# Kernel tuning notes

Hardware: AMD Instinct MI355X
Metric: run time of the kernel (lower is better)

Reference implementation:

```python
import jax, jax.numpy as jnp
import numpy as np

N_NODES = 50000


def gcn_conv(x, W, b, src, dst, ew, n_nodes):
    """PyG GCNConv: out = D^{-1/2}(A + I)D^{-1/2} (x @ W) + b, A weighted by ew.

    Self loops (weight 1) are handled analytically instead of appending edges.
    """
    h = x @ W  # [N, out]
    # degree includes self-loop weight of 1
    deg = jax.ops.segment_sum(ew, dst, num_segments=n_nodes) + 1.0  # [N]
    dinv = jnp.where(deg > 0, jax.lax.rsqrt(deg), 0.0)
    norm = dinv[src] * ew * dinv[dst]  # [E]
    # message = norm * h[src], scatter-add to dst
    agg = jax.ops.segment_sum(h[src] * norm[:, None], dst, num_segments=n_nodes)
    # self-loop contribution: dinv[i] * 1 * dinv[i] * h[i]
    agg = agg + h * (dinv * dinv)[:, None]
    return agg + b


def setup_inputs() -> dict:
    key = jax.random.key(0)
    k = jax.random.split(key, 8)
    n, e, d_in, d_h = N_NODES, 600000, 128, 128
    x = jax.random.normal(k[0], (n, d_in), dtype=jnp.float32)
    edge_index = jax.random.randint(k[1], (2, e), 0, n, dtype=jnp.int64)
    edge_attr = jax.random.uniform(k[2], (e,), dtype=jnp.float32)
    s1 = 1.0 / np.sqrt(d_in)
    s2 = 1.0 / np.sqrt(d_h)
    W1 = jax.random.uniform(k[3], (d_in, d_h), jnp.float32, -s1, s1)
    b1 = jnp.zeros((d_h,), jnp.float32)
    W2 = jax.random.uniform(k[4], (d_h, d_h), jnp.float32, -s2, s2)
    b2 = jnp.zeros((d_h,), jnp.float32)
    return {"x": x, "edge_index": edge_index, "edge_attr": edge_attr,
            "W1": W1, "b1": b1, "W2": W2, "b2": b2}


def reference(x, edge_index, edge_attr, W1, b1, W2, b2):
    src, dst = edge_index[0], edge_index[1]
    h = gcn_conv(x, W1, b1, src, dst, edge_attr, N_NODES)
    h = jax.nn.relu(h)
    # dropout is identity in eval mode (deterministic reference)
    out = gcn_conv(h, W2, b2, src, dst, edge_attr, N_NODES)
    return out
```

## Files before the change

### kernel.cpp

```cpp
#include <hip/hip_runtime.h>
#include <stdint.h>

#define D 128
#define EPB 4096
#define CSZ 128

typedef __bf16 bf16x8 __attribute__((ext_vector_type(8)));
typedef float f32x4 __attribute__((ext_vector_type(4)));

__device__ inline float bf2f(unsigned short u) {
    return __uint_as_float((unsigned)u << 16);
}
__device__ inline unsigned short f2bf(float f) {
    unsigned u = __float_as_uint(f);
    return (unsigned short)((u + 0x7FFF + ((u >> 16) & 1)) >> 16);
}

struct Params {
    const float* x; const int* ei; const float* ew;
    const float* W1; const float* b1; const float* W2; const float* b2;
    float* out;
    int N, E, C, B1n, total, gb, hb, sb;
    unsigned short *Wt1, *Wt2;
    unsigned int* bh; int* ebase; int* bsums;
    float* dinv; int* cnt; int* rowstart;
    int2* brec; int2* erec;
    unsigned short *Hbuf, *Abuf;
};


__device__ inline void dev_prep(int which, const Params& p) {
    const float* W = (which == 0) ? p.W1 : p.W2;
    unsigned short* Wt = (which == 0) ? p.Wt1 : p.Wt2;
    for (int i = threadIdx.x; i < 2048; i += 256) {
        int nn = i >> 4;
        int kc = (i & 15) << 3;
        ushort4 o0, o1;
        o0.x = f2bf(W[(kc + 0) * 128 + nn]); o0.y = f2bf(W[(kc + 1) * 128 + nn]);
        o0.z = f2bf(W[(kc + 2) * 128 + nn]); o0.w = f2bf(W[(kc + 3) * 128 + nn]);
        o1.x = f2bf(W[(kc + 4) * 128 + nn]); o1.y = f2bf(W[(kc + 5) * 128 + nn]);
        o1.z = f2bf(W[(kc + 6) * 128 + nn]); o1.w = f2bf(W[(kc + 7) * 128 + nn]);
        *(ushort4*)(Wt + nn * 128 + kc) = o0;
        *(ushort4*)(Wt + nn * 128 + kc + 4) = o1;
    }
}

__device__ inline void dev_hist(int b, const Params& p, unsigned int* hist) {
    for (int i = threadIdx.x; i < p.C; i += 256) hist[i] = 0;
    __syncthreads();
    const int base = b * EPB + threadIdx.x;
#pragma unroll
    for (int k = 0; k < EPB / 256; ++k) {
        int e = base + k * 256;
        if (e < p.E) atomicAdd(&hist[((unsigned)p.ei[p.E + e]) >> 7], 1u);
    }
    __syncthreads();
    for (int i = threadIdx.x; i < p.C; i += 256) p.bh[(size_t)b * p.C + i] = hist[i];
}

__device__ inline void dev_scanA(int blk, const Params& p, int* tmp) {
    const int tid = threadIdx.x;
    const int i = blk * 256 + tid;
    int v = 0;
    if (i < p.total) {
        int c = i / p.B1n;
        int b = i - c * p.B1n;
        v = (int)p.bh[(size_t)b * p.C + c];
    }
    tmp[tid] = v;
    __syncthreads();
    for (int off = 1; off < 256; off <<= 1) {
        int t = (tid >= off) ? tmp[tid - off] : 0;
        __syncthreads();
        tmp[tid] += t;
        __syncthreads();
    }
    if (i < p.total) p.ebase[i] = tmp[tid] - v;
    if (tid == 255) p.bsums[blk] = tmp[255];
}

__device__ inline void dev_scanB(int blk, const Params& p, int* sred) {
    const int tid = threadIdx.x;
    int v = (tid < blk) ? p.bsums[tid] : 0;
#pragma unroll
    for (int off = 32; off; off >>= 1) v += __shfl_down(v, off);
    if ((tid & 63) == 0) sred[tid >> 6] = v;
    __syncthreads();
    int tot = sred[0] + sred[1] + sred[2] + sred[3];
    int i = blk * 256 + tid;
    if (i < p.total) p.ebase[i] += tot;
}

__device__ inline void dev_scat(int b, const Params& p, unsigned int* cur) {
    for (int i = threadIdx.x; i < p.C; i += 256) cur[i] = 0;
    __syncthreads();
    const int base = b * EPB + threadIdx.x;
#pragma unroll
    for (int k = 0; k < EPB / 256; ++k) {
        int e = base + k * 256;
        if (e < p.E) {
            int s = p.ei[e];
            unsigned d = (unsigned)p.ei[p.E + e];
            float w = p.ew[e];
            int c = d >> 7;
            unsigned r = atomicAdd(&cur[c], 1u);
            int pos = p.ebase[c * p.B1n + b] + (int)r;
            p.brec[pos] = make_int2((int)((d << 16) | (unsigned)s), __float_as_int(w));
        }
    }
}

__device__ inline void dev_cbuild(int c, const Params& p, unsigned int* a) {
    unsigned int* hcnt = a;
    unsigned int* hdeg = a + CSZ;
    unsigned int* lsc  = a + 2 * CSZ;
    unsigned int* curs = a + 3 * CSZ;
    const int tid = threadIdx.x;
    const int cs = p.ebase[c * p.B1n];
    const int ce = (c + 1 < p.C) ? p.ebase[(c + 1) * p.B1n] : p.E;
    if (tid < CSZ) { hcnt[tid] = 0; hdeg[tid] = 0; }
    __syncthreads();
    for (int i = cs + tid; i < ce; i += 256) {
        int2 r = p.brec[i];
        int local = (int)(((unsigned)r.x) >> 16) & (CSZ - 1);
        atomicAdd(&hcnt[local], 1u);
        atomicAdd(&hdeg[local], (unsigned)(__int_as_float(r.y) * 16777216.0f));
    }
    __syncthreads();
    if (tid < CSZ) lsc[tid] = hcnt[tid];
    __syncthreads();
    for (int off = 1; off < CSZ; off <<= 1) {
        unsigned t = (tid < CSZ && tid >= off) ? lsc[tid - off] : 0u;
        __syncthreads();
        if (tid < CSZ) lsc[tid] += t;
        __syncthreads();
    }
    if (tid < CSZ) {
        unsigned excl = lsc[tid] - hcnt[tid];
        curs[tid] = excl;
        int node = c * CSZ + tid;
        if (node < p.N) {
            p.rowstart[node] = cs + (int)excl;
            p.cnt[node] = (int)hcnt[tid];
            float deg = 1.0f + (float)hdeg[tid] * (1.0f / 16777216.0f);
            p.dinv[node] = rsqrtf(deg);
        }
    }
    __syncthreads();
    for (int i = cs + tid; i < ce; i += 256) {
        int2 r = p.brec[i];
        int local = (int)(((unsigned)r.x) >> 16) & (CSZ - 1);
        unsigned rk = atomicAdd(&curs[local], 1u);
        p.erec[cs + (int)rk] = make_int2(r.x & 0xFFFF, r.y);
    }
}

template <bool IN_BF16>
__device__ inline void mfma_body(unsigned short* sE,
                                 const void* __restrict__ Xv,
                                 const unsigned short* __restrict__ Wt,
                                 unsigned short* __restrict__ H, int n, int blk) {
    const int tid = threadIdx.x;
    const int row0 = blk * 64;
    const int lane = tid & 63;
    const int wv = tid >> 6;
    const int qm = lane & 15;
    const int quad = lane >> 4;

    const int arow = row0 + wv * 16 + qm;
    const int ar = (arow < n) ? arow : (n - 1);

    f32x4 acc[8];
#pragma unroll
    for (int i = 0; i < 8; ++i) acc[i] = (f32x4){0.f, 0.f, 0.f, 0.f};

#pragma unroll
    for (int kb = 0; kb < 4; ++kb) {
        const int koff = kb * 32 + quad * 8;
        bf16x8 a;
        if (IN_BF16) {
            a = *(const bf16x8*)((const unsigned short*)Xv + (size_t)ar * 128 + koff);
        } else {
            const float* Xf = (const float*)Xv + (size_t)ar * 128 + koff;
            float4 v0 = *(const float4*)(Xf);
            float4 v1 = *(const float4*)(Xf + 4);
            union { bf16x8 v; ushort4 u[2]; } cv;
            cv.u[0].x = f2bf(v0.x); cv.u[0].y = f2bf(v0.y);
            cv.u[0].z = f2bf(v0.z); cv.u[0].w = f2bf(v0.w);
            cv.u[1].x = f2bf(v1.x); cv.u[1].y = f2bf(v1.y);
            cv.u[1].z = f2bf(v1.z); cv.u[1].w = f2bf(v1.w);
            a = cv.v;
        }
#pragma unroll
        for (int n0 = 0; n0 < 8; ++n0) {
            bf16x8 b = *(const bf16x8*)(Wt + (n0 * 16 + qm) * 128 + koff);
            acc[n0] = __builtin_amdgcn_mfma_f32_16x16x32_bf16(a, b, acc[n0], 0, 0, 0);
        }
    }

#pragma unroll
    for (int n0 = 0; n0 < 8; ++n0)
#pragma unroll
        for (int r = 0; r < 4; ++r)
            sE[(wv * 16 + quad * 4 + r) * 136 + n0 * 16 + qm] = f2bf(acc[n0][r]);
    __syncthreads();

    const int row_in = lane >> 2;
    const int c0 = (lane & 3) * 4;
    const int grow = row0 + wv * 16 + row_in;
    if (grow < n) {
#pragma unroll
        for (int j = 0; j < 4; ++j)
            *(int4*)(H + (size_t)grow * 128 + (c0 + j) * 8) =
                *(const int4*)(&sE[(wv * 16 + row_in) * 136 + (c0 + j) * 8]);
    }
}

template <bool OUT_BF16>
__device__ inline void gather_body(const Params& p, const ushort4* __restrict__ H4,
                                   const float4* __restrict__ bias4,
                                   void* __restrict__ OUTv, int g) {
    const int lane = threadIdx.x & 31;
    const int node = g * 8 + (threadIdx.x >> 5);
    if (node >= p.N) return;
    const int start = p.rowstart[node];
    const int m = p.cnt[node];
    const float di = p.dinv[node];

    float4 b = bias4[lane];
    ushort4 h = H4[(size_t)node * 32 + lane];
    float ax = di * bf2f(h.x);
    float ay = di * bf2f(h.y);
    float az = di * bf2f(h.z);
    float aw = di * bf2f(h.w);

    int j = 0;
    for (; j + 4 <= m; j += 4) {
        const int base = start + j;
        int2 e0 = p.erec[base + 0], e1 = p.erec[base + 1];
        int2 e2 = p.erec[base + 2], e3 = p.erec[base + 3];
        float w0 = p.dinv[e0.x] * __int_as_float(e0.y);
        float w1 = p.dinv[e1.x] * __int_as_float(e1.y);
        float w2 = p.dinv[e2.x] * __int_as_float(e2.y);
        float w3 = p.dinv[e3.x] * __int_as_float(e3.y);
        ushort4 v0 = H4[(size_t)e0.x * 32 + lane];
        ushort4 v1 = H4[(size_t)e1.x * 32 + lane];
        ushort4 v2 = H4[(size_t)e2.x * 32 + lane];
        ushort4 v3 = H4[(size_t)e3.x * 32 + lane];
        ax += w0 * bf2f(v0.x); ay += w0 * bf2f(v0.y); az += w0 * bf2f(v0.z); aw += w0 * bf2f(v0.w);
        ax += w1 * bf2f(v1.x); ay += w1 * bf2f(v1.y); az += w1 * bf2f(v1.z); aw += w1 * bf2f(v1.w);
        ax += w2 * bf2f(v2.x); ay += w2 * bf2f(v2.y); az += w2 * bf2f(v2.z); aw += w2 * bf2f(v2.w);
        ax += w3 * bf2f(v3.x); ay += w3 * bf2f(v3.y); az += w3 * bf2f(v3.z); aw += w3 * bf2f(v3.w);
    }
    for (; j < m; ++j) {
        int2 er = p.erec[start + j];
        float w = p.dinv[er.x] * __int_as_float(er.y);
        ushort4 v = H4[(size_t)er.x * 32 + lane];
        ax += w * bf2f(v.x); ay += w * bf2f(v.y); az += w * bf2f(v.z); aw += w * bf2f(v.w);
    }
    ax = b.x + di * ax; ay = b.y + di * ay;
    az = b.z + di * az; aw = b.w + di * aw;
    if (OUT_BF16) {
        ushort4 o;
        o.x = f2bf(fmaxf(ax, 0.f)); o.y = f2bf(fmaxf(ay, 0.f));
        o.z = f2bf(fmaxf(az, 0.f)); o.w = f2bf(fmaxf(aw, 0.f));
        ((ushort4*)OUTv)[(size_t)node * 32 + lane] = o;
    } else {
        float4 o; o.x = ax; o.y = ay; o.z = az; o.w = aw;
        ((float4*)OUTv)[(size_t)node * 32 + lane] = o;
    }
}

__global__ __launch_bounds__(256, 4) void k_f0(Params p) {
    __shared__ __align__(16) char arena[64 * 136 * 2];
    if (blockIdx.x < 2) dev_prep(blockIdx.x, p);
    else dev_hist(blockIdx.x - 2, p, (unsigned int*)arena);
}
__global__ __launch_bounds__(256, 4) void k_f1(Params p) {
    __shared__ __align__(16) char arena[64 * 136 * 2];
    if ((int)blockIdx.x < p.gb) mfma_body<false>((unsigned short*)arena, (const void*)p.x, p.Wt1, p.Hbuf, p.N, blockIdx.x);
    else dev_scanA(blockIdx.x - p.gb, p, (int*)arena);
}
__global__ __launch_bounds__(256) void k_f2(Params p) {
    __shared__ int sred[4];
    dev_scanB(blockIdx.x, p, sred);
}
__global__ __launch_bounds__(256) void k_f3(Params p) {
    __shared__ unsigned int cur[512];
    dev_scat(blockIdx.x, p, cur);
}
__global__ __launch_bounds__(256) void k_f4(Params p) {
    __shared__ unsigned int a[4 * CSZ];
    dev_cbuild(blockIdx.x, p, a);
}
__global__ __launch_bounds__(256) void k_f5(Params p) {
    gather_body<true>(p, (const ushort4*)p.Hbuf, (const float4*)p.b1, (void*)p.Abuf, blockIdx.x);
}
__global__ __launch_bounds__(256, 4) void k_f6(Params p) {
    __shared__ __align__(16) char arena[64 * 136 * 2];
    mfma_body<true>((unsigned short*)arena, (const void*)p.Abuf, p.Wt2, p.Hbuf, p.N, blockIdx.x);
}
__global__ __launch_bounds__(256) void k_f7(Params p) {
    gather_body<false>(p, (const ushort4*)p.Hbuf, (const float4*)p.b2, (void*)p.out, blockIdx.x);
}

extern "C" void kernel_launch(void* const* d_in, const int* in_sizes, int n_in,
                              void* d_out, int out_size, void* d_ws, size_t ws_size,
                              hipStream_t stream) {
    Params p;
    p.x  = (const float*)d_in[0];
    p.ei = (const int*)d_in[1];
    p.ew = (const float*)d_in[2];
    p.W1 = (const float*)d_in[3];
    p.b1 = (const float*)d_in[4];
    p.W2 = (const float*)d_in[5];
    p.b2 = (const float*)d_in[6];
    p.out = (float*)d_out;

    p.N = in_sizes[0] / D;
    p.E = in_sizes[2];
    p.C = (p.N + CSZ - 1) / CSZ;
    p.B1n = (p.E + EPB - 1) / EPB;
    p.total = p.C * p.B1n;
    p.sb = (p.total + 255) / 256;
    p.gb = (p.N + 63) / 64;
    p.hb = (p.N + 7) / 8;

    char* w = (char*)d_ws;
    auto alloc = [&](size_t bytes) {
        void* r = (void*)w;
        w += (bytes + 255) & ~(size_t)255;
        return r;
    };
    p.bh       = (unsigned int*)alloc((size_t)p.total * 4);
    p.ebase    = (int*)alloc((size_t)p.total * 4);
    p.bsums    = (int*)alloc(1024 * 4);
    p.dinv     = (float*)alloc((size_t)p.N * 4);
    p.cnt      = (int*)alloc((size_t)p.N * 4);
    p.rowstart = (int*)alloc((size_t)p.N * 4);
    p.brec     = (int2*)alloc((size_t)p.E * 8);
    p.erec     = (int2*)alloc((size_t)p.E * 8);
    p.Hbuf     = (unsigned short*)alloc((size_t)p.N * D * 2);
    p.Abuf     = (unsigned short*)alloc((size_t)p.N * D * 2);
    p.Wt1      = (unsigned short*)alloc(128 * 128 * 2);
    p.Wt2      = (unsigned short*)alloc(128 * 128 * 2);

    k_f0<<<2 + p.B1n, 256, 0, stream>>>(p);
    k_f1<<<p.gb + p.sb, 256, 0, stream>>>(p);
    k_f2<<<p.sb, 256, 0, stream>>>(p);
    k_f3<<<p.B1n, 256, 0, stream>>>(p);
    k_f4<<<p.C, 256, 0, stream>>>(p);
    k_f5<<<p.hb, 256, 0, stream>>>(p);
    k_f6<<<p.gb, 256, 0, stream>>>(p);
    k_f7<<<p.hb, 256, 0, stream>>>(p);
}
```

Baseline: 218.8 us.

## Fuse all GCN stages into one cooperative persistent kernel with grid syncs

Replaces the eight separate kernel launches with a single cooperative kernel that loops over work units per stage and separates stages with grid-wide barriers. The bucketing step is rebuilt around a global per-chunk counter, a scan in a single block, and atomic cursor allocation, which removes the large per-block histogram scan. The goal is to cut launch gaps and the cost of the multi-pass scan. In exchange it adds grid.sync overhead, a fixed persistent grid size, and non-deterministic edge ordering inside each bucket. The old launch sequence stays as a fallback if the cooperative launch fails.

```diff
diff --git a/kernel.cpp b/kernel.cpp
--- a/kernel.cpp
+++ b/kernel.cpp
@@ -1,8 +1,12 @@
 #include <hip/hip_runtime.h>
+#include <hip/hip_cooperative_groups.h>
 #include <stdint.h>
+
+namespace cg = cooperative_groups;
 
 #define D 128
 #define EPB 4096
+#define EPB2 1024
 #define CSZ 128
 
 typedef __bf16 bf16x8 __attribute__((ext_vector_type(8)));
@@ -20,9 +24,10 @@
     const float* x; const int* ei; const float* ew;
     const float* W1; const float* b1; const float* W2; const float* b2;
     float* out;
-    int N, E, C, B1n, total, gb, hb, sb;
+    int N, E, C, B1n, B2n, total, gb, hb, sb;
     unsigned short *Wt1, *Wt2;
     unsigned int* bh; int* ebase; int* bsums;
+    unsigned int* ctot; int* cbase; unsigned int* gcur;
     float* dinv; int* cnt; int* rowstart;
     int2* brec; int2* erec;
     unsigned short *Hbuf, *Abuf;
@@ -110,14 +115,78 @@
     }
 }
 
-__device__ inline void dev_cbuild(int c, const Params& p, unsigned int* a) {
+__device__ inline void dev_hist2(int b, const Params& p, unsigned int* hist) {
+    for (int i = threadIdx.x; i < p.C; i += 256) hist[i] = 0;
+    __syncthreads();
+    const int base = b * EPB2 + threadIdx.x;
+#pragma unroll
+    for (int k = 0; k < EPB2 / 256; ++k) {
+        int e = base + k * 256;
+        if (e < p.E) atomicAdd(&hist[((unsigned)p.ei[p.E + e]) >> 7], 1u);
+    }
+    __syncthreads();
+    for (int i = threadIdx.x; i < p.C; i += 256) {
+        unsigned v = hist[i];
+        if (v) atomicAdd(&p.ctot[i], v);
+    }
+}
+
+__device__ inline void dev_cscan(const Params& p, int* s) {
+    const int tid = threadIdx.x;
+    const int c0 = tid, c1 = tid + 256;
+    s[c0] = (c0 < p.C) ? (int)p.ctot[c0] : 0;
+    s[c1] = (c1 < p.C) ? (int)p.ctot[c1] : 0;
+    __syncthreads();
+    for (int off = 1; off < 512; off <<= 1) {
+        int t0 = (c0 >= off) ? s[c0 - off] : 0;
+        int t1 = (c1 >= off) ? s[c1 - off] : 0;
+        __syncthreads();
+        s[c0] += t0; s[c1] += t1;
+        __syncthreads();
+    }
+    if (c0 < p.C) { int b0 = (c0 == 0) ? 0 : s[c0 - 1]; p.cbase[c0] = b0; p.gcur[c0] = (unsigned)b0; }
+    if (c1 < p.C) { int b1 = s[c1 - 1]; p.cbase[c1] = b1; p.gcur[c1] = (unsigned)b1; }
+    if (tid == 0) p.cbase[p.C] = p.E;
+}
+
+__device__ inline void dev_scat2(int b, const Params& p, unsigned int* a) {
+    unsigned int* hcnt = a;
+    unsigned int* hcur = a + 512;
+    const int tid = threadIdx.x;
+    for (int i = tid; i < p.C; i += 256) hcnt[i] = 0;
+    __syncthreads();
+    const int base = b * EPB2 + tid;
+#pragma unroll
+    for (int k = 0; k < EPB2 / 256; ++k) {
+        int e = base + k * 256;
+        if (e < p.E) atomicAdd(&hcnt[((unsigned)p.ei[p.E + e]) >> 7], 1u);
+    }
+    __syncthreads();
+    for (int i = tid; i < p.C; i += 256) {
+        unsigned c = hcnt[i];
+        hcur[i] = c ? atomicAdd(&p.gcur[i], c) : 0u;
+    }
+    __syncthreads();
+#pragma unroll
+    for (int k = 0; k < EPB2 / 256; ++k) {
+        int e = base + k * 256;
+        if (e < p.E) {
+            int s = p.ei[e];
+            unsigned d = (unsigned)p.ei[p.E + e];
+            float w = p.ew[e];
+            int c = (int)(d >> 7);
+            unsigned r = atomicAdd(&hcur[c], 1u);
+            p.brec[r] = make_int2((int)((d << 16) | (unsigned)s), __float_as_int(w));
+        }
+    }
+}
+
+__device__ inline void dev_cbuild(int c, const Params& p, unsigned int* a, int cs, int ce) {
     unsigned int* hcnt = a;
     unsigned int* hdeg = a + CSZ;
     unsigned int* lsc  = a + 2 * CSZ;
     unsigned int* curs = a + 3 * CSZ;
     const int tid = threadIdx.x;
-    const int cs = p.ebase[c * p.B1n];
-    const int ce = (c + 1 < p.C) ? p.ebase[(c + 1) * p.B1n] : p.E;
     if (tid < CSZ) { hcnt[tid] = 0; hdeg[tid] = 0; }
     __syncthreads();
     for (int i = cs + tid; i < ce; i += 256) {
@@ -222,53 +291,99 @@
                                    void* __restrict__ OUTv, int g) {
     const int lane = threadIdx.x & 31;
     const int node = g * 8 + (threadIdx.x >> 5);
-    if (node >= p.N) return;
-    const int start = p.rowstart[node];
-    const int m = p.cnt[node];
-    const float di = p.dinv[node];
-
-    float4 b = bias4[lane];
-    ushort4 h = H4[(size_t)node * 32 + lane];
-    float ax = di * bf2f(h.x);
-    float ay = di * bf2f(h.y);
-    float az = di * bf2f(h.z);
-    float aw = di * bf2f(h.w);
-
-    int j = 0;
-    for (; j + 4 <= m; j += 4) {
-        const int base = start + j;
-        int2 e0 = p.erec[base + 0], e1 = p.erec[base + 1];
-        int2 e2 = p.erec[base + 2], e3 = p.erec[base + 3];
-        float w0 = p.dinv[e0.x] * __int_as_float(e0.y);
-        float w1 = p.dinv[e1.x] * __int_as_float(e1.y);
-        float w2 = p.dinv[e2.x] * __int_as_float(e2.y);
-        float w3 = p.dinv[e3.x] * __int_as_float(e3.y);
-        ushort4 v0 = H4[(size_t)e0.x * 32 + lane];
-        ushort4 v1 = H4[(size_t)e1.x * 32 + lane];
-        ushort4 v2 = H4[(size_t)e2.x * 32 + lane];
-        ushort4 v3 = H4[(size_t)e3.x * 32 + lane];
-        ax += w0 * bf2f(v0.x); ay += w0 * bf2f(v0.y); az += w0 * bf2f(v0.z); aw += w0 * bf2f(v0.w);
-        ax += w1 * bf2f(v1.x); ay += w1 * bf2f(v1.y); az += w1 * bf2f(v1.z); aw += w1 * bf2f(v1.w);
-        ax += w2 * bf2f(v2.x); ay += w2 * bf2f(v2.y); az += w2 * bf2f(v2.z); aw += w2 * bf2f(v2.w);
-        ax += w3 * bf2f(v3.x); ay += w3 * bf2f(v3.y); az += w3 * bf2f(v3.z); aw += w3 * bf2f(v3.w);
-    }
-    for (; j < m; ++j) {
-        int2 er = p.erec[start + j];
-        float w = p.dinv[er.x] * __int_as_float(er.y);
-        ushort4 v = H4[(size_t)er.x * 32 + lane];
-        ax += w * bf2f(v.x); ay += w * bf2f(v.y); az += w * bf2f(v.z); aw += w * bf2f(v.w);
-    }
-    ax = b.x + di * ax; ay = b.y + di * ay;
-    az = b.z + di * az; aw = b.w + di * aw;
-    if (OUT_BF16) {
-        ushort4 o;
-        o.x = f2bf(fmaxf(ax, 0.f)); o.y = f2bf(fmaxf(ay, 0.f));
-        o.z = f2bf(fmaxf(az, 0.f)); o.w = f2bf(fmaxf(aw, 0.f));
-        ((ushort4*)OUTv)[(size_t)node * 32 + lane] = o;
-    } else {
-        float4 o; o.x = ax; o.y = ay; o.z = az; o.w = aw;
-        ((float4*)OUTv)[(size_t)node * 32 + lane] = o;
-    }
+    if (node < p.N) {
+        const int start = p.rowstart[node];
+        const int m = p.cnt[node];
+        const float di = p.dinv[node];
+
+        float4 b = bias4[lane];
+        ushort4 h = H4[(size_t)node * 32 + lane];
+        float ax = di * bf2f(h.x);
+        float ay = di * bf2f(h.y);
+        float az = di * bf2f(h.z);
+        float aw = di * bf2f(h.w);
+
+        int j = 0;
+        for (; j + 4 <= m; j += 4) {
+            const int base = start + j;
+            int2 e0 = p.erec[base + 0], e1 = p.erec[base + 1];
+            int2 e2 = p.erec[base + 2], e3 = p.erec[base + 3];
+            float w0 = p.dinv[e0.x] * __int_as_float(e0.y);
+            float w1 = p.dinv[e1.x] * __int_as_float(e1.y);
+            float w2 = p.dinv[e2.x] * __int_as_float(e2.y);
+            float w3 = p.dinv[e3.x] * __int_as_float(e3.y);
+            ushort4 v0 = H4[(size_t)e0.x * 32 + lane];
+            ushort4 v1 = H4[(size_t)e1.x * 32 + lane];
+            ushort4 v2 = H4[(size_t)e2.x * 32 + lane];
+            ushort4 v3 = H4[(size_t)e3.x * 32 + lane];
+            ax += w0 * bf2f(v0.x); ay += w0 * bf2f(v0.y); az += w0 * bf2f(v0.z); aw += w0 * bf2f(v0.w);
+            ax += w1 * bf2f(v1.x); ay += w1 * bf2f(v1.y); az += w1 * bf2f(v1.z); aw += w1 * bf2f(v1.w);
+            ax += w2 * bf2f(v2.x); ay += w2 * bf2f(v2.y); az += w2 * bf2f(v2.z); aw += w2 * bf2f(v2.w);
+            ax += w3 * bf2f(v3.x); ay += w3 * bf2f(v3.y); az += w3 * bf2f(v3.z); aw += w3 * bf2f(v3.w);
+        }
+        for (; j < m; ++j) {
+            int2 er = p.erec[start + j];
+            float w = p.dinv[er.x] * __int_as_float(er.y);
+            ushort4 v = H4[(size_t)er.x * 32 + lane];
+            ax += w * bf2f(v.x); ay += w * bf2f(v.y); az += w * bf2f(v.z); aw += w * bf2f(v.w);
+        }
+        ax = b.x + di * ax; ay = b.y + di * ay;
+        az = b.z + di * az; aw = b.w + di * aw;
+        if (OUT_BF16) {
+            ushort4 o;
+            o.x = f2bf(fmaxf(ax, 0.f)); o.y = f2bf(fmaxf(ay, 0.f));
+            o.z = f2bf(fmaxf(az, 0.f)); o.w = f2bf(fmaxf(aw, 0.f));
+            ((ushort4*)OUTv)[(size_t)node * 32 + lane] = o;
+        } else {
+            float4 o; o.x = ax; o.y = ay; o.z = az; o.w = aw;
+            ((float4*)OUTv)[(size_t)node * 32 + lane] = o;
+        }
+    }
+}
+
+__global__ __launch_bounds__(256, 4) void k_all(Params p) {
+    __shared__ __align__(16) char arena[64 * 136 * 2];
+    cg::grid_group grid = cg::this_grid();
+    const int nb = (int)gridDim.x;
+
+    for (int u = blockIdx.x; u < 2 + p.B2n; u += nb) {
+        if (u < 2) dev_prep(u, p);
+        else dev_hist2(u - 2, p, (unsigned int*)arena);
+        __syncthreads();
+    }
+    grid.sync();
+
+    for (int u = blockIdx.x; u < p.gb + 1; u += nb) {
+        if (u < p.gb) mfma_body<false>((unsigned short*)arena, (const void*)p.x, p.Wt1, p.Hbuf, p.N, u);
+        else dev_cscan(p, (int*)arena);
+        __syncthreads();
+    }
+    grid.sync();
+
+    for (int u = blockIdx.x; u < p.B2n; u += nb) {
+        dev_scat2(u, p, (unsigned int*)arena);
+        __syncthreads();
+    }
+    grid.sync();
+
+    for (int u = blockIdx.x; u < p.C; u += nb) {
+        dev_cbuild(u, p, (unsigned int*)arena, p.cbase[u], p.cbase[u + 1]);
+        __syncthreads();
+    }
+    grid.sync();
+
+    for (int u = blockIdx.x; u < p.hb; u += nb)
+        gather_body<true>(p, (const ushort4*)p.Hbuf, (const float4*)p.b1, (void*)p.Abuf, u);
+    grid.sync();
+
+    for (int u = blockIdx.x; u < p.gb; u += nb) {
+        mfma_body<true>((unsigned short*)arena, (const void*)p.Abuf, p.Wt2, p.Hbuf, p.N, u);
+        __syncthreads();
+    }
+    grid.sync();
+
+    for (int u = blockIdx.x; u < p.hb; u += nb)
+        gather_body<false>(p, (const ushort4*)p.Hbuf, (const float4*)p.b2, (void*)p.out, u);
 }
 
 __global__ __launch_bounds__(256, 4) void k_f0(Params p) {
@@ -291,7 +406,10 @@
 }
 __global__ __launch_bounds__(256) void k_f4(Params p) {
     __shared__ unsigned int a[4 * CSZ];
-    dev_cbuild(blockIdx.x, p, a);
+    int c = blockIdx.x;
+    int cs = p.ebase[c * p.B1n];
+    int ce = (c + 1 < p.C) ? p.ebase[(c + 1) * p.B1n] : p.E;
+    dev_cbuild(c, p, a, cs, ce);
 }
 __global__ __launch_bounds__(256) void k_f5(Params p) {
     gather_body<true>(p, (const ushort4*)p.Hbuf, (const float4*)p.b1, (void*)p.Abuf, blockIdx.x);
@@ -321,6 +439,7 @@
     p.E = in_sizes[2];
     p.C = (p.N + CSZ - 1) / CSZ;
     p.B1n = (p.E + EPB - 1) / EPB;
+    p.B2n = (p.E + EPB2 - 1) / EPB2;
     p.total = p.C * p.B1n;
     p.sb = (p.total + 255) / 256;
     p.gb = (p.N + 63) / 64;
@@ -335,6 +454,9 @@
     p.bh       = (unsigned int*)alloc((size_t)p.total * 4);
     p.ebase    = (int*)alloc((size_t)p.total * 4);
     p.bsums    = (int*)alloc(1024 * 4);
+    p.ctot     = (unsigned int*)alloc((size_t)p.C * 4);
+    p.cbase    = (int*)alloc((size_t)(p.C + 1) * 4);
+    p.gcur     = (unsigned int*)alloc((size_t)p.C * 4);
     p.dinv     = (float*)alloc((size_t)p.N * 4);
     p.cnt      = (int*)alloc((size_t)p.N * 4);
     p.rowstart = (int*)alloc((size_t)p.N * 4);
@@ -345,12 +467,38 @@
     p.Wt1      = (unsigned short*)alloc(128 * 128 * 2);
     p.Wt2      = (unsigned short*)alloc(128 * 128 * 2);
 
-    k_f0<<<2 + p.B1n, 256, 0, stream>>>(p);
-    k_f1<<<p.gb + p.sb, 256, 0, stream>>>(p);
-    k_f2<<<p.sb, 256, 0, stream>>>(p);
-    k_f3<<<p.B1n, 256, 0, stream>>>(p);
-    k_f4<<<p.C, 256, 0, stream>>>(p);
-    k_f5<<<p.hb, 256, 0, stream>>>(p);
-    k_f6<<<p.gb, 256, 0, stream>>>(p);
-    k_f7<<<p.hb, 256, 0, stream>>>(p);
-}
+    bool fused_ok = (p.C <= 512);
+
+    static int s_grid = 0;
+    if (s_grid == 0) {
+        int ba = 0;
+        if (hipOccupancyMaxActiveBlocksPerMultiprocessor(&ba, (const void*)k_all, 256, 0) != hipSuccess || ba < 1)
+            ba = 2;
+        int ncu = 256;
+        hipDeviceProp_t prop;
+        int dev = 0;
+        if (hipGetDevice(&dev) == hipSuccess && hipGetDeviceProperties(&prop, dev) == hipSuccess &&
+            prop.multiProcessorCount > 0)
+            ncu = prop.multiProcessorCount;
+        long g = (long)ba * (long)ncu;
+        s_grid = (int)(g > 1024 ? 1024 : g);
+        if (s_grid < 64) s_grid = 64;
+    }
+
+    hipError_t err = hipErrorUnknown;
+    if (fused_ok) {
+        hipMemsetAsync(p.ctot, 0, (size_t)p.C * 4, stream);
+        void* kargs[] = { (void*)&p };
+        err = hipLaunchCooperativeKernel((const void*)k_all, dim3(s_grid), dim3(256), kargs, 0u, stream);
+    }
+    if (err != hipSuccess) {
+        k_f0<<<2 + p.B1n, 256, 0, stream>>>(p);
+        k_f1<<<p.gb + p.sb, 256, 0, stream>>>(p);
+        k_f2<<<p.sb, 256, 0, stream>>>(p);
+        k_f3<<<p.B1n, 256, 0, stream>>>(p);
+        k_f4<<<p.C, 256, 0, stream>>>(p);
+        k_f5<<<p.hb, 256, 0, stream>>>(p);
+        k_f6<<<p.gb, 256, 0, stream>>>(p);
+        k_f7<<<p.hb, 256, 0, stream>>>(p);
+    }
+}
```

New measurement: 680.9 us. 3.11x slower.

## Replace two-level bucket scan with global atomic cursors and fuse gather1 into GEMM2

Applied to the files above, without the earlier changes.

The per-block histogram scan (scanA/scanB, two launches) is replaced by per-bucket totals accumulated with global atomics, a single-block scan, and a scatter that reserves ranges through global atomic cursors. The scatter recounts its own edges to get its reservation. The first-layer aggregation now writes straight into LDS and feeds the second-layer MFMA GEMM in the same kernel, so the intermediate activation buffer no longer round-trips through global memory and two launches are removed. Edge order within a bucket now depends on atomic timing, so float sums are no longer deterministic. The fused kernel uses 8 threads per node, which may lower gather parallelism and occupancy.

```diff
diff --git a/kernel.cpp b/kernel.cpp
--- a/kernel.cpp
+++ b/kernel.cpp
@@ -2,7 +2,7 @@
 #include <stdint.h>
 
 #define D 128
-#define EPB 4096
+#define EPB2 1024
 #define CSZ 128
 
 typedef __bf16 bf16x8 __attribute__((ext_vector_type(8)));
@@ -20,12 +20,12 @@
     const float* x; const int* ei; const float* ew;
     const float* W1; const float* b1; const float* W2; const float* b2;
     float* out;
-    int N, E, C, B1n, total, gb, hb, sb;
+    int N, E, C, B2n, gb, hb;
     unsigned short *Wt1, *Wt2;
-    unsigned int* bh; int* ebase; int* bsums;
+    unsigned int* ctot; int* cbase; unsigned int* gcur;
     float* dinv; int* cnt; int* rowstart;
     int2* brec; int2* erec;
-    unsigned short *Hbuf, *Abuf;
+    unsigned short *Hbuf, *H2;
 };
 
 
@@ -45,79 +45,78 @@
     }
 }
 
-__device__ inline void dev_hist(int b, const Params& p, unsigned int* hist) {
+__device__ inline void dev_hist2(int b, const Params& p, unsigned int* hist) {
     for (int i = threadIdx.x; i < p.C; i += 256) hist[i] = 0;
     __syncthreads();
-    const int base = b * EPB + threadIdx.x;
-#pragma unroll
-    for (int k = 0; k < EPB / 256; ++k) {
+    const int base = b * EPB2 + threadIdx.x;
+#pragma unroll
+    for (int k = 0; k < EPB2 / 256; ++k) {
         int e = base + k * 256;
         if (e < p.E) atomicAdd(&hist[((unsigned)p.ei[p.E + e]) >> 7], 1u);
     }
     __syncthreads();
-    for (int i = threadIdx.x; i < p.C; i += 256) p.bh[(size_t)b * p.C + i] = hist[i];
-}
-
-__device__ inline void dev_scanA(int blk, const Params& p, int* tmp) {
-    const int tid = threadIdx.x;
-    const int i = blk * 256 + tid;
-    int v = 0;
-    if (i < p.total) {
-        int c = i / p.B1n;
-        int b = i - c * p.B1n;
-        v = (int)p.bh[(size_t)b * p.C + c];
-    }
-    tmp[tid] = v;
-    __syncthreads();
-    for (int off = 1; off < 256; off <<= 1) {
-        int t = (tid >= off) ? tmp[tid - off] : 0;
+    for (int i = threadIdx.x; i < p.C; i += 256) {
+        unsigned v = hist[i];
+        if (v) atomicAdd(&p.ctot[i], v);
+    }
+}
+
+__device__ inline void dev_cscan(const Params& p, int* s) {
+    const int tid = threadIdx.x;
+    const int c0 = tid, c1 = tid + 256;
+    s[c0] = (c0 < p.C) ? (int)p.ctot[c0] : 0;
+    s[c1] = (c1 < p.C) ? (int)p.ctot[c1] : 0;
+    __syncthreads();
+    for (int off = 1; off < 512; off <<= 1) {
+        int t0 = (c0 >= off) ? s[c0 - off] : 0;
+        int t1 = (c1 >= off) ? s[c1 - off] : 0;
         __syncthreads();
-        tmp[tid] += t;
+        s[c0] += t0; s[c1] += t1;
         __syncthreads();
     }
-    if (i < p.total) p.ebase[i] = tmp[tid] - v;
-    if (tid == 255) p.bsums[blk] = tmp[255];
-}
-
-__device__ inline void dev_scanB(int blk, const Params& p, int* sred) {
-    const int tid = threadIdx.x;
-    int v = (tid < blk) ? p.bsums[tid] : 0;
-#pragma unroll
-    for (int off = 32; off; off >>= 1) v += __shfl_down(v, off);
-    if ((tid & 63) == 0) sred[tid >> 6] = v;
-    __syncthreads();
-    int tot = sred[0] + sred[1] + sred[2] + sred[3];
-    int i = blk * 256 + tid;
-    if (i < p.total) p.ebase[i] += tot;
-}
-
-__device__ inline void dev_scat(int b, const Params& p, unsigned int* cur) {
-    for (int i = threadIdx.x; i < p.C; i += 256) cur[i] = 0;
-    __syncthreads();
-    const int base = b * EPB + threadIdx.x;
-#pragma unroll
-    for (int k = 0; k < EPB / 256; ++k) {
+    if (c0 < p.C) { int b0 = (c0 == 0) ? 0 : s[c0 - 1]; p.cbase[c0] = b0; p.gcur[c0] = (unsigned)b0; }
+    if (c1 < p.C) { int b1 = s[c1 - 1]; p.cbase[c1] = b1; p.gcur[c1] = (unsigned)b1; }
+    if (tid == 0) p.cbase[p.C] = p.E;
+}
+
+__device__ inline void dev_scat2(int b, const Params& p, unsigned int* a) {
+    unsigned int* hcnt = a;
+    unsigned int* hcur = a + 512;
+    const int tid = threadIdx.x;
+    for (int i = tid; i < p.C; i += 256) hcnt[i] = 0;
+    __syncthreads();
+    const int base = b * EPB2 + tid;
+#pragma unroll
+    for (int k = 0; k < EPB2 / 256; ++k) {
+        int e = base + k * 256;
+        if (e < p.E) atomicAdd(&hcnt[((unsigned)p.ei[p.E + e]) >> 7], 1u);
+    }
+    __syncthreads();
+    for (int i = tid; i < p.C; i += 256) {
+        unsigned c = hcnt[i];
+        hcur[i] = c ? atomicAdd(&p.gcur[i], c) : 0u;
+    }
+    __syncthreads();
+#pragma unroll
+    for (int k = 0; k < EPB2 / 256; ++k) {
         int e = base + k * 256;
         if (e < p.E) {
             int s = p.ei[e];
             unsigned d = (unsigned)p.ei[p.E + e];
             float w = p.ew[e];
-            int c = d >> 7;
-            unsigned r = atomicAdd(&cur[c], 1u);
-            int pos = p.ebase[c * p.B1n + b] + (int)r;
-            p.brec[pos] = make_int2((int)((d << 16) | (unsigned)s), __float_as_int(w));
-        }
-    }
-}
-
-__device__ inline void dev_cbuild(int c, const Params& p, unsigned int* a) {
+            int c = (int)(d >> 7);
+            unsigned r = atomicAdd(&hcur[c], 1u);
+            p.brec[r] = make_int2((int)((d << 16) | (unsigned)s), __float_as_int(w));
+        }
+    }
+}
+
+__device__ inline void dev_cbuild(int c, const Params& p, unsigned int* a, int cs, int ce) {
     unsigned int* hcnt = a;
     unsigned int* hdeg = a + CSZ;
     unsigned int* lsc  = a + 2 * CSZ;
     unsigned int* curs = a + 3 * CSZ;
     const int tid = threadIdx.x;
-    const int cs = p.ebase[c * p.B1n];
-    const int ce = (c + 1 < p.C) ? p.ebase[(c + 1) * p.B1n] : p.E;
     if (tid < CSZ) { hcnt[tid] = 0; hdeg[tid] = 0; }
     __syncthreads();
     for (int i = cs + tid; i < ce; i += 256) {
@@ -216,10 +215,81 @@
     }
 }
 
-template <bool OUT_BF16>
-__device__ inline void gather_body(const Params& p, const ushort4* __restrict__ H4,
-                                   const float4* __restrict__ bias4,
-                                   void* __restrict__ OUTv, int g) {
+__device__ inline void gather1_to_lds(const Params& p, unsigned short* sA, int row0) {
+    const int tid = threadIdx.x;
+    const int lane8 = tid & 7;
+    const int grp = tid >> 3;
+    const ushort4* __restrict__ H4 = (const ushort4*)p.Hbuf;
+#pragma unroll
+    for (int pass = 0; pass < 2; ++pass) {
+        const int local = pass * 32 + grp;
+        const int node = row0 + local;
+        unsigned short* dst = sA + local * 136 + lane8 * 16;
+        if (node < p.N) {
+            const int start = p.rowstart[node];
+            const int m = p.cnt[node];
+            const float di = p.dinv[node];
+            const ushort4* Hrow = H4 + (size_t)node * 32 + lane8 * 4;
+            float acc[16];
+#pragma unroll
+            for (int q = 0; q < 4; ++q) {
+                ushort4 h = Hrow[q];
+                acc[q * 4 + 0] = di * bf2f(h.x);
+                acc[q * 4 + 1] = di * bf2f(h.y);
+                acc[q * 4 + 2] = di * bf2f(h.z);
+                acc[q * 4 + 3] = di * bf2f(h.w);
+            }
+            int j = 0;
+            for (; j + 2 <= m; j += 2) {
+                int2 e0 = p.erec[start + j];
+                int2 e1 = p.erec[start + j + 1];
+                float w0 = p.dinv[e0.x] * __int_as_float(e0.y);
+                float w1 = p.dinv[e1.x] * __int_as_float(e1.y);
+                const ushort4* V0 = H4 + (size_t)e0.x * 32 + lane8 * 4;
+                const ushort4* V1 = H4 + (size_t)e1.x * 32 + lane8 * 4;
+#pragma unroll
+                for (int q = 0; q < 4; ++q) {
+                    ushort4 v0 = V0[q], v1 = V1[q];
+                    acc[q * 4 + 0] += w0 * bf2f(v0.x) + w1 * bf2f(v1.x);
+                    acc[q * 4 + 1] += w0 * bf2f(v0.y) + w1 * bf2f(v1.y);
+                    acc[q * 4 + 2] += w0 * bf2f(v0.z) + w1 * bf2f(v1.z);
+                    acc[q * 4 + 3] += w0 * bf2f(v0.w) + w1 * bf2f(v1.w);
+                }
+            }
+            if (j < m) {
+                int2 e0 = p.erec[start + j];
+                float w0 = p.dinv[e0.x] * __int_as_float(e0.y);
+                const ushort4* V0 = H4 + (size_t)e0.x * 32 + lane8 * 4;
+#pragma unroll
+                for (int q = 0; q < 4; ++q) {
+                    ushort4 v0 = V0[q];
+                    acc[q * 4 + 0] += w0 * bf2f(v0.x);
+                    acc[q * 4 + 1] += w0 * bf2f(v0.y);
+                    acc[q * 4 + 2] += w0 * bf2f(v0.z);
+                    acc[q * 4 + 3] += w0 * bf2f(v0.w);
+                }
+            }
+            const float* bb = p.b1 + lane8 * 16;
+#pragma unroll
+            for (int q = 0; q < 4; ++q) {
+                ushort4 o;
+                o.x = f2bf(fmaxf(bb[q * 4 + 0] + di * acc[q * 4 + 0], 0.f));
+                o.y = f2bf(fmaxf(bb[q * 4 + 1] + di * acc[q * 4 + 1], 0.f));
+                o.z = f2bf(fmaxf(bb[q * 4 + 2] + di * acc[q * 4 + 2], 0.f));
+                o.w = f2bf(fmaxf(bb[q * 4 + 3] + di * acc[q * 4 + 3], 0.f));
+                *(ushort4*)(dst + q * 4) = o;
+            }
+        } else {
+            ushort4 z = {0, 0, 0, 0};
+#pragma unroll
+            for (int q = 0; q < 4; ++q) *(ushort4*)(dst + q * 4) = z;
+        }
+    }
+}
+
+__device__ inline void gather2_body(const Params& p, const ushort4* __restrict__ H4,
+                                    const float4* __restrict__ bias4,
+                                    float4* __restrict__ OUT, int g) {
     const int lane = threadIdx.x & 31;
     const int node = g * 8 + (threadIdx.x >> 5);
     if (node >= p.N) return;
@@ -258,50 +328,77 @@
         ushort4 v = H4[(size_t)er.x * 32 + lane];
         ax += w * bf2f(v.x); ay += w * bf2f(v.y); az += w * bf2f(v.z); aw += w * bf2f(v.w);
     }
-    ax = b.x + di * ax; ay = b.y + di * ay;
-    az = b.z + di * az; aw = b.w + di * aw;
-    if (OUT_BF16) {
-        ushort4 o;
-        o.x = f2bf(fmaxf(ax, 0.f)); o.y = f2bf(fmaxf(ay, 0.f));
-        o.z = f2bf(fmaxf(az, 0.f)); o.w = f2bf(fmaxf(aw, 0.f));
-        ((ushort4*)OUTv)[(size_t)node * 32 + lane] = o;
-    } else {
-        float4 o; o.x = ax; o.y = ay; o.z = az; o.w = aw;
-        ((float4*)OUTv)[(size_t)node * 32 + lane] = o;
-    }
-}
-
-__global__ __launch_bounds__(256, 4) void k_f0(Params p) {
-    __shared__ __align__(16) char arena[64 * 136 * 2];
+    float4 o;
+    o.x = b.x + di * ax; o.y = b.y + di * ay;
+    o.z = b.z + di * az; o.w = b.w + di * aw;
+    OUT[(size_t)node * 32 + lane] = o;
+}
+
+__global__ __launch_bounds__(256, 4) void k_a0(Params p) {
+    __shared__ __align__(16) unsigned int hist[512];
     if (blockIdx.x < 2) dev_prep(blockIdx.x, p);
-    else dev_hist(blockIdx.x - 2, p, (unsigned int*)arena);
-}
-__global__ __launch_bounds__(256, 4) void k_f1(Params p) {
+    else dev_hist2(blockIdx.x - 2, p, hist);
+}
+__global__ __launch_bounds__(256, 4) void k_a1(Params p) {
     __shared__ __align__(16) char arena[64 * 136 * 2];
     if ((int)blockIdx.x < p.gb) mfma_body<false>((unsigned short*)arena, (const void*)p.x, p.Wt1, p.Hbuf, p.N, blockIdx.x);
-    else dev_scanA(blockIdx.x - p.gb, p, (int*)arena);
-}
-__global__ __launch_bounds__(256) void k_f2(Params p) {
-    __shared__ int sred[4];
-    dev_scanB(blockIdx.x, p, sred);
-}
-__global__ __launch_bounds__(256) void k_f3(Params p) {
-    __shared__ unsigned int cur[512];
-    dev_scat(blockIdx.x, p, cur);
-}
-__global__ __launch_bounds__(256) void k_f4(Params p) {
+    else dev_cscan(p, (int*)arena);
+}
+__global__ __launch_bounds__(256) void k_a2(Params p) {
+    __shared__ unsigned int a[1024];
+    dev_scat2(blockIdx.x, p, a);
+}
+__global__ __launch_bounds__(256) void k_a3(Params p) {
     __shared__ unsigned int a[4 * CSZ];
-    dev_cbuild(blockIdx.x, p, a);
-}
-__global__ __launch_bounds__(256) void k_f5(Params p) {
-    gather_body<true>(p, (const ushort4*)p.Hbuf, (const float4*)p.b1, (void*)p.Abuf, blockIdx.x);
-}
-__global__ __launch_bounds__(256, 4) void k_f6(Params p) {
-    __shared__ __align__(16) char arena[64 * 136 * 2];
-    mfma_body<true>((unsigned short*)arena, (const void*)p.Abuf, p.Wt2, p.Hbuf, p.N, blockIdx.x);
-}
-__global__ __launch_bounds__(256) void k_f7(Params p) {
-    gather_body<false>(p, (const ushort4*)p.Hbuf, (const float4*)p.b2, (void*)p.out, blockIdx.x);
+    dev_cbuild(blockIdx.x, p, a, p.cbase[blockIdx.x], p.cbase[blockIdx.x + 1]);
+}
+__global__ __launch_bounds__(256, 4) void k_a4(Params p) {
+    __shared__ __align__(16) unsigned short sA[64 * 136];
+    __shared__ __align__(16) unsigned short sE[64 * 136];
+    const int row0 = blockIdx.x * 64;
+    gather1_to_lds(p, sA, row0);
+    __syncthreads();
+
+    const int tid = threadIdx.x;
+    const int lane = tid & 63;
+    const int wv = tid >> 6;
+    const int qm = lane & 15;
+    const int quad = lane >> 4;
+
+    f32x4 acc[8];
+#pragma unroll
+    for (int i = 0; i < 8; ++i) acc[i] = (f32x4){0.f, 0.f, 0.f, 0.f};
+
+#pragma unroll
+    for (int kb = 0; kb < 4; ++kb) {
+        const int koff = kb * 32 + quad * 8;
+        bf16x8 a = *(const bf16x8*)(sA + (wv * 16 + qm) * 136 + koff);
+#pragma unroll
+        for (int n0 = 0; n0 < 8; ++n0) {
+            bf16x8 b = *(const bf16x8*)(p.Wt2 + (n0 * 16 + qm) * 128 + koff);
+            acc[n0] = __builtin_amdgcn_mfma_f32_16x16x32_bf16(a, b, acc[n0], 0, 0, 0);
+        }
+    }
+
+#pragma unroll
+    for (int n0 = 0; n0 < 8; ++n0)
+#pragma unroll
+        for (int r = 0; r < 4; ++r)
+            sE[(wv * 16 + quad * 4 + r) * 136 + n0 * 16 + qm] = f2bf(acc[n0][r]);
+    __syncthreads();
+
+    const int row_in = lane >> 2;
+    const int c0 = (lane & 3) * 4;
+    const int grow = row0 + wv * 16 + row_in;
+    if (grow < p.N) {
+#pragma unroll
+        for (int j = 0; j < 4; ++j)
+            *(int4*)(p.H2 + (size_t)grow * 128 + (c0 + j) * 8) =
+                *(const int4*)(&sE[(wv * 16 + row_in) * 136 + (c0 + j) * 8]);
+    }
+}
+__global__ __launch_bounds__(256) void k_a5(Params p) {
+    gather2_body(p, (const ushort4*)p.H2, (const float4*)p.b2, (float4*)p.out, blockIdx.x);
 }
 
 extern "C" void kernel_launch(void* const* d_in, const int* in_sizes, int n_in,
@@ -320,9 +417,7 @@
     p.N = in_sizes[0] / D;
     p.E = in_sizes[2];
     p.C = (p.N + CSZ - 1) / CSZ;
-    p.B1n = (p.E + EPB - 1) / EPB;
-    p.total = p.C * p.B1n;
-    p.sb = (p.total + 255) / 256;
+    p.B2n = (p.E + EPB2 - 1) / EPB2;
     p.gb = (p.N + 63) / 64;
     p.hb = (p.N + 7) / 8;
 
@@ -332,25 +427,24 @@
         w += (bytes + 255) & ~(size_t)255;
         return r;
     };
-    p.bh       = (unsigned int*)alloc((size_t)p.total * 4);
-    p.ebase    = (int*)alloc((size_t)p.total * 4);
-    p.bsums    = (int*)alloc(1024 * 4);
+    p.ctot     = (unsigned int*)alloc((size_t)p.C * 4);
+    p.cbase    = (int*)alloc((size_t)(p.C + 1) * 4);
+    p.gcur     = (unsigned int*)alloc((size_t)p.C * 4);
     p.dinv     = (float*)alloc((size_t)p.N * 4);
     p.cnt      = (int*)alloc((size_t)p.N * 4);
     p.rowstart = (int*)alloc((size_t)p.N * 4);
     p.brec     = (int2*)alloc((size_t)p.E * 8);
     p.erec     = (int2*)alloc((size_t)p.E * 8);
     p.Hbuf     = (unsigned short*)alloc((size_t)p.N * D * 2);
-    p.Abuf     = (unsigned short*)alloc((size_t)p.N * D * 2);
+    p.H2       = (unsigned short*)alloc((size_t)p.N * D * 2);
     p.Wt1      = (unsigned short*)alloc(128 * 128 * 2);
     p.Wt2      = (unsigned short*)alloc(128 * 128 * 2);
 
-    k_f0<<<2 + p.B1n, 256, 0, stream>>>(p);
-    k_f1<<<p.gb + p.sb, 256, 0, stream>>>(p);
-    k_f2<<<p.sb, 256, 0, stream>>>(p);
-    k_f3<<<p.B1n, 256, 0, stream>>>(p);
-    k_f4<<<p.C, 256, 0, stream>>>(p);
-    k_f5<<<p.hb, 256, 0, stream>>>(p);
-    k_f6<<<p.gb, 256, 0, stream>>>(p);
-    k_f7<<<p.hb, 256, 0, stream>>>(p);
-}
+    hipMemsetAsync(p.ctot, 0, (size_t)p.C * 4, stream);
+    k_a0<<<2 + p.B2n, 256, 0, stream>>>(p);
+    k_a1<<<p.gb + 1, 256, 0, stream>>>(p);
+    k_a2<<<p.B2n, 256, 0, stream>>>(p);
+    k_a3<<<p.C, 256, 0, stream>>>(p);
+    k_a4<<<p.gb, 256, 0, stream>>>(p);
+    k_a5<<<p.hb, 256, 0, stream>>>(p);
+}
```

After: 227.5 us. 1.04x slower.

## Replace two-level bucketed CSR build with per-node global atomic counting sort

Applied to the files above, without the earlier changes.

The two-pass bucket sort (per-block chunk histograms, two-level scan, bucket scatter, per-chunk local rebuild) is replaced by per-destination global atomics. One packed 64-bit atomic accumulates both edge count and degree per node, a per-node scan plus a single-block scan of block sums builds row offsets, and one scatter pass places edges through per-node atomic cursors. This removes the intermediate brec buffer and one kernel, but adds a memset and relies on heavy global atomics and a serial single-block scan. Edge order within each row becomes nondeterministic.

```diff
diff --git a/kernel.cpp b/kernel.cpp
--- a/kernel.cpp
+++ b/kernel.cpp
@@ -2,8 +2,7 @@
 #include <stdint.h>
 
 #define D 128
-#define EPB 4096
-#define CSZ 128
+#define EPB 1024
 
 typedef __bf16 bf16x8 __attribute__((ext_vector_type(8)));
 typedef float f32x4 __attribute__((ext_vector_type(4)));
@@ -20,11 +19,15 @@
     const float* x; const int* ei; const float* ew;
     const float* W1; const float* b1; const float* W2; const float* b2;
     float* out;
-    int N, E, C, B1n, total, gb, hb, sb;
+    int N, E, hbn, gb, hb, sn;
     unsigned short *Wt1, *Wt2;
-    unsigned int* bh; int* ebase; int* bsums;
-    float* dinv; int* cnt; int* rowstart;
-    int2* brec; int2* erec;
+    unsigned long long* cntdeg;
+    unsigned int* cur;
+    int* lbase;
+    int* cnt;
+    float* dinv;
+    int* bsum; int* bpref;
+    int2* erec;
     unsigned short *Hbuf, *Abuf;
 };
 
@@ -45,29 +48,32 @@
     }
 }
 
-__device__ inline void dev_hist(int b, const Params& p, unsigned int* hist) {
-    for (int i = threadIdx.x; i < p.C; i += 256) hist[i] = 0;
-    __syncthreads();
+__device__ inline void dev_hist(int b, const Params& p) {
     const int base = b * EPB + threadIdx.x;
 #pragma unroll
     for (int k = 0; k < EPB / 256; ++k) {
         int e = base + k * 256;
-        if (e < p.E) atomicAdd(&hist[((unsigned)p.ei[p.E + e]) >> 7], 1u);
-    }
-    __syncthreads();
-    for (int i = threadIdx.x; i < p.C; i += 256) p.bh[(size_t)b * p.C + i] = hist[i];
-}
-
-__device__ inline void dev_scanA(int blk, const Params& p, int* tmp) {
+        if (e < p.E) {
+            unsigned d = (unsigned)p.ei[p.E + e];
+            unsigned long long pk =
+                (1ULL << 40) | (unsigned long long)(unsigned)(p.ew[e] * 16777216.0f);
+            atomicAdd(&p.cntdeg[d], pk);
+        }
+    }
+}
+
+__device__ inline void dev_scanL(int b, const Params& p, int* tmp) {
     const int tid = threadIdx.x;
-    const int i = blk * 256 + tid;
-    int v = 0;
-    if (i < p.total) {
-        int c = i / p.B1n;
-        int b = i - c * p.B1n;
-        v = (int)p.bh[(size_t)b * p.C + c];
-    }
-    tmp[tid] = v;
+    const int n = b * 256 + tid;
+    int c = 0;
+    if (n < p.N) {
+        unsigned long long v = p.cntdeg[n];
+        c = (int)(v >> 40);
+        float deg = 1.0f + (float)(v & 0xFFFFFFFFFFULL) * (1.0f / 16777216.0f);
+        p.dinv[n] = rsqrtf(deg);
+        p.cnt[n] = c;
+    }
+    tmp[tid] = c;
     __syncthreads();
     for (int off = 1; off < 256; off <<= 1) {
         int t = (tid >= off) ? tmp[tid - off] : 0;
@@ -75,25 +81,11 @@
         tmp[tid] += t;
         __syncthreads();
     }
-    if (i < p.total) p.ebase[i] = tmp[tid] - v;
-    if (tid == 255) p.bsums[blk] = tmp[255];
-}
-
-__device__ inline void dev_scanB(int blk, const Params& p, int* sred) {
-    const int tid = threadIdx.x;
-    int v = (tid < blk) ? p.bsums[tid] : 0;
-#pragma unroll
-    for (int off = 32; off; off >>= 1) v += __shfl_down(v, off);
-    if ((tid & 63) == 0) sred[tid >> 6] = v;
-    __syncthreads();
-    int tot = sred[0] + sred[1] + sred[2] + sred[3];
-    int i = blk * 256 + tid;
-    if (i < p.total) p.ebase[i] += tot;
-}
-
-__device__ inline void dev_scat(int b, const Params& p, unsigned int* cur) {
-    for (int i = threadIdx.x; i < p.C; i += 256) cur[i] = 0;
-    __syncthreads();
+    if (n < p.N) p.lbase[n] = tmp[tid] - c;
+    if (tid == 255) p.bsum[b] = tmp[255];
+}
+
+__device__ inline void dev_scat(int b, const Params& p) {
     const int base = b * EPB + threadIdx.x;
 #pragma unroll
     for (int k = 0; k < EPB / 256; ++k) {
@@ -102,56 +94,9 @@
             int s = p.ei[e];
             unsigned d = (unsigned)p.ei[p.E + e];
             float w = p.ew[e];
-            int c = d >> 7;
-            unsigned r = atomicAdd(&cur[c], 1u);
-            int pos = p.ebase[c * p.B1n + b] + (int)r;
-            p.brec[pos] = make_int2((int)((d << 16) | (unsigned)s), __float_as_int(w));
-        }
-    }
-}
-
-__device__ inline void dev_cbuild(int c, const Params& p, unsigned int* a) {
-    unsigned int* hcnt = a;
-    unsigned int* hdeg = a + CSZ;
-    unsigned int* lsc  = a + 2 * CSZ;
-    unsigned int* curs = a + 3 * CSZ;
-    const int tid = threadIdx.x;
-    const int cs = p.ebase[c * p.B1n];
-    const int ce = (c + 1 < p.C) ? p.ebase[(c + 1) * p.B1n] : p.E;
-    if (tid < CSZ) { hcnt[tid] = 0; hdeg[tid] = 0; }
-    __syncthreads();
-    for (int i = cs + tid; i < ce; i += 256) {
-        int2 r = p.brec[i];
-        int local = (int)(((unsigned)r.x) >> 16) & (CSZ - 1);
-        atomicAdd(&hcnt[local], 1u);
-        atomicAdd(&hdeg[local], (unsigned)(__int_as_float(r.y) * 16777216.0f));
-    }
-    __syncthreads();
-    if (tid < CSZ) lsc[tid] = hcnt[tid];
-    __syncthreads();
-    for (int off = 1; off < CSZ; off <<= 1) {
-        unsigned t = (tid < CSZ && tid >= off) ? lsc[tid - off] : 0u;
-        __syncthreads();
-        if (tid < CSZ) lsc[tid] += t;
-        __syncthreads();
-    }
-    if (tid < CSZ) {
-        unsigned excl = lsc[tid] - hcnt[tid];
-        curs[tid] = excl;
-        int node = c * CSZ + tid;
-        if (node < p.N) {
-            p.rowstart[node] = cs + (int)excl;
-            p.cnt[node] = (int)hcnt[tid];
-            float deg = 1.0f + (float)hdeg[tid] * (1.0f / 16777216.0f);
-            p.dinv[node] = rsqrtf(deg);
-        }
-    }
-    __syncthreads();
-    for (int i = cs + tid; i < ce; i += 256) {
-        int2 r = p.brec[i];
-        int local = (int)(((unsigned)r.x) >> 16) & (CSZ - 1);
-        unsigned rk = atomicAdd(&curs[local], 1u);
-        p.erec[cs + (int)rk] = make_int2(r.x & 0xFFFF, r.y);
+            int pos = p.lbase[d] + p.bpref[d >> 8] + (int)atomicAdd(&p.cur[d], 1u);
+            p.erec[pos] = make_int2(s, __float_as_int(w));
+        }
     }
 }
 
@@ -223,7 +168,7 @@
     const int lane = threadIdx.x & 31;
     const int node = g * 8 + (threadIdx.x >> 5);
     if (node >= p.N) return;
-    const int start = p.rowstart[node];
+    const int start = p.lbase[node] + p.bpref[node >> 8];
     const int m = p.cnt[node];
     const float di = p.dinv[node];
 
@@ -271,36 +216,51 @@
     }
 }
 
-__global__ __launch_bounds__(256, 4) void k_f0(Params p) {
+__global__ __launch_bounds__(256, 4) void k_c0(Params p) {
+    if (blockIdx.x < 2) dev_prep(blockIdx.x, p);
+    else dev_hist(blockIdx.x - 2, p);
+}
+__global__ __launch_bounds__(256, 4) void k_c1(Params p) {
     __shared__ __align__(16) char arena[64 * 136 * 2];
-    if (blockIdx.x < 2) dev_prep(blockIdx.x, p);
-    else dev_hist(blockIdx.x - 2, p, (unsigned int*)arena);
-}
-__global__ __launch_bounds__(256, 4) void k_f1(Params p) {
-    __shared__ __align__(16) char arena[64 * 136 * 2];
-    if ((int)blockIdx.x < p.gb) mfma_body<false>((unsigned short*)arena, (const void*)p.x, p.Wt1, p.Hbuf, p.N, blockIdx.x);
-    else dev_scanA(blockIdx.x - p.gb, p, (int*)arena);
-}
-__global__ __launch_bounds__(256) void k_f2(Params p) {
-    __shared__ int sred[4];
-    dev_scanB(blockIdx.x, p, sred);
-}
-__global__ __launch_bounds__(256) void k_f3(Params p) {
-    __shared__ unsigned int cur[512];
-    dev_scat(blockIdx.x, p, cur);
-}
-__global__ __launch_bounds__(256) void k_f4(Params p) {
-    __shared__ unsigned int a[4 * CSZ];
-    dev_cbuild(blockIdx.x, p, a);
-}
-__global__ __launch_bounds__(256) void k_f5(Params p) {
+    if ((int)blockIdx.x < p.gb)
+        mfma_body<false>((unsigned short*)arena, (const void*)p.x, p.Wt1, p.Hbuf, p.N, blockIdx.x);
+    else
+        dev_scanL(blockIdx.x - p.gb, p, (int*)arena);
+}
+__global__ __launch_bounds__(256) void k_c2(Params p) {
+    __shared__ int tmp[256];
+    __shared__ int carry;
+    const int tid = threadIdx.x;
+    if (tid == 0) carry = 0;
+    __syncthreads();
+    for (int base = 0; base < p.sn; base += 256) {
+        int i = base + tid;
+        int v = (i < p.sn) ? p.bsum[i] : 0;
+        tmp[tid] = v;
+        __syncthreads();
+        for (int off = 1; off < 256; off <<= 1) {
+            int t = (tid >= off) ? tmp[tid - off] : 0;
+            __syncthreads();
+            tmp[tid] += t;
+            __syncthreads();
+        }
+        if (i < p.sn) p.bpref[i] = carry + tmp[tid] - v;
+        __syncthreads();
+        if (tid == 0) carry += tmp[255];
+        __syncthreads();
+    }
+}
+__global__ __launch_bounds__(256) void k_c3(Params p) {
+    dev_scat(blockIdx.x, p);
+}
+__global__ __launch_bounds__(256) void k_c4(Params p) {
     gather_body<true>(p, (const ushort4*)p.Hbuf, (const float4*)p.b1, (void*)p.Abuf, blockIdx.x);
 }
-__global__ __launch_bounds__(256, 4) void k_f6(Params p) {
+__global__ __launch_bounds__(256, 4) void k_c5(Params p) {
     __shared__ __align__(16) char arena[64 * 136 * 2];
     mfma_body<true>((unsigned short*)arena, (const void*)p.Abuf, p.Wt2, p.Hbuf, p.N, blockIdx.x);
 }
-__global__ __launch_bounds__(256) void k_f7(Params p) {
+__global__ __launch_bounds__(256) void k_c6(Params p) {
     gather_body<false>(p, (const ushort4*)p.Hbuf, (const float4*)p.b2, (void*)p.out, blockIdx.x);
 }
 
@@ -319,12 +279,10 @@
 
     p.N = in_sizes[0] / D;
     p.E = in_sizes[2];
-    p.C = (p.N + CSZ - 1) / CSZ;
-    p.B1n = (p.E + EPB - 1) / EPB;
-    p.total = p.C * p.B1n;
-    p.sb = (p.total + 255) / 256;
+    p.hbn = (p.E + EPB - 1) / EPB;
     p.gb = (p.N + 63) / 64;
     p.hb = (p.N + 7) / 8;
+    p.sn = (p.N + 255) / 256;
 
     char* w = (char*)d_ws;
     auto alloc = [&](size_t bytes) {
@@ -332,25 +290,27 @@
         w += (bytes + 255) & ~(size_t)255;
         return r;
     };
-    p.bh       = (unsigned int*)alloc((size_t)p.total * 4);
-    p.ebase    = (int*)alloc((size_t)p.total * 4);
-    p.bsums    = (int*)alloc(1024 * 4);
+    p.cntdeg   = (unsigned long long*)alloc((size_t)p.N * 8);
+    p.cur      = (unsigned int*)alloc((size_t)p.N * 4);
+    p.lbase    = (int*)alloc((size_t)p.N * 4);
+    p.cnt      = (int*)alloc((size_t)p.N * 4);
     p.dinv     = (float*)alloc((size_t)p.N * 4);
-    p.cnt      = (int*)alloc((size_t)p.N * 4);
-    p.rowstart = (int*)alloc((size_t)p.N * 4);
-    p.brec     = (int2*)alloc((size_t)p.E * 8);
+    p.bsum     = (int*)alloc((size_t)(p.sn + 1) * 4);
+    p.bpref    = (int*)alloc((size_t)(p.sn + 1) * 4);
     p.erec     = (int2*)alloc((size_t)p.E * 8);
     p.Hbuf     = (unsigned short*)alloc((size_t)p.N * D * 2);
     p.Abuf     = (unsigned short*)alloc((size_t)p.N * D * 2);
     p.Wt1      = (unsigned short*)alloc(128 * 128 * 2);
     p.Wt2      = (unsigned short*)alloc(128 * 128 * 2);
 
-    k_f0<<<2 + p.B1n, 256, 0, stream>>>(p);
-    k_f1<<<p.gb + p.sb, 256, 0, stream>>>(p);
-    k_f2<<<p.sb, 256, 0, stream>>>(p);
-    k_f3<<<p.B1n, 256, 0, stream>>>(p);
-    k_f4<<<p.C, 256, 0, stream>>>(p);
-    k_f5<<<p.hb, 256, 0, stream>>>(p);
-    k_f6<<<p.gb, 256, 0, stream>>>(p);
-    k_f7<<<p.hb, 256, 0, stream>>>(p);
-}
+    size_t zspan = (size_t)((char*)p.cur - (char*)p.cntdeg) + (size_t)p.N * 4;
+    hipMemsetAsync(p.cntdeg, 0, zspan, stream);
+
+    k_c0<<<2 + p.hbn, 256, 0, stream>>>(p);
+    k_c1<<<p.gb + p.sn, 256, 0, stream>>>(p);
+    k_c2<<<1, 256, 0, stream>>>(p);
+    k_c3<<<p.hbn, 256, 0, stream>>>(p);
+    k_c4<<<p.hb, 256, 0, stream>>>(p);
+    k_c5<<<p.gb, 256, 0, stream>>>(p);
+    k_c6<<<p.hb, 256, 0, stream>>>(p);
+}
```

Measured after the change: 257.2 us. +17.6%, slower.
